# Performance work log

Measured on AMD Instinct MI355X. Metric: run time of the kernel, lower is better.

## Reference

```python
import jax, jax.numpy as jnp
import numpy as np
from jax import lax

D_MODEL, D_INNER, D_STATE, DT_RANK, KG, DCONV = 96, 96, 64, 6, 4, 3
BATCH, SEQ = 4, 16384


def setup_inputs() -> dict:
    ks = jax.random.split(jax.random.key(0), 8)
    x = jax.random.normal(ks[0], (BATCH, SEQ, D_MODEL), jnp.float32)
    in_proj_w = jax.random.normal(ks[1], (2 * D_INNER, D_MODEL), jnp.float32) * (D_MODEL ** -0.5)
    conv_w = jax.random.normal(ks[2], (D_INNER, 1, DCONV), jnp.float32) * (DCONV ** -0.5)
    x_proj_w = jax.random.normal(ks[3], (KG, DT_RANK + 2 * D_STATE, D_INNER), jnp.float32) * (D_INNER ** -0.5)
    dt_projs_w = 0.1 * jax.random.uniform(ks[4], (KG, D_INNER, DT_RANK), jnp.float32)
    out_proj_w = jax.random.normal(ks[5], (D_MODEL, D_INNER), jnp.float32) * (D_INNER ** -0.5)
    A_logs = 0.1 * jax.random.uniform(ks[6], (KG * D_INNER, D_STATE), jnp.float32)
    Ds = jnp.ones((KG * D_INNER,), jnp.float32)
    return dict(x=x, in_proj_w=in_proj_w, conv_w=conv_w, x_proj_w=x_proj_w,
                dt_projs_w=dt_projs_w, out_proj_w=out_proj_w, A_logs=A_logs, Ds=Ds)


def _forward_core(x, x_proj_w, dt_projs_w, A_logs, Ds):
    # x: (B, L, Din). 4-direction stack: [fwd, rev, fwd, rev] as in torch code.
    B, L, Din = x.shape
    x_rev = jnp.flip(x, axis=1)
    xs = jnp.stack([x, x_rev, x, x_rev], axis=1)                      # (B, K, L, Din)
    x_dbl = jnp.einsum('bkld,kcd->bklc', xs, x_proj_w)                # (B, K, L, R+2N)
    dts, Bs, Cs = jnp.split(x_dbl, [DT_RANK, DT_RANK + D_STATE], axis=-1)
    dts = jnp.einsum('bklr,kdr->bkld', dts, dt_projs_w)               # (B, K, L, Din)
    delta = jax.nn.softplus(dts)                                      # delta_bias is zeros in source
    A = -jnp.exp(A_logs).reshape(KG, D_INNER, D_STATE)                # (K, Din, N)
    D = Ds.reshape(KG, D_INNER)

    def step(h, inp):
        d, u, b, c = inp                                              # d,u:(B,K,Din)  b,c:(B,K,N)
        dA = jnp.exp(d[..., None] * A)                                # (B,K,Din,N)
        h = dA * h + (d * u)[..., None] * b[:, :, None, :]
        y = jnp.einsum('bkdn,bkn->bkd', h, c)
        return h, y

    seq = (jnp.moveaxis(delta, 2, 0), jnp.moveaxis(xs, 2, 0),
           jnp.moveaxis(Bs, 2, 0), jnp.moveaxis(Cs, 2, 0))
    h0 = jnp.zeros((B, KG, D_INNER, D_STATE), x.dtype)
    _, ys = lax.scan(step, h0, seq)                                   # (L, B, K, Din)
    ys = jnp.moveaxis(ys, 0, 2) + D[None, :, None, :] * xs            # (B, K, L, Din)
    # cross-merge: un-flip the reversed directions and sum all 4
    y = ys[:, 0] + jnp.flip(ys[:, 1], axis=1) + ys[:, 2] + jnp.flip(ys[:, 3], axis=1)
    return y                                                          # (B, L, Din)


def reference(x, in_proj_w, conv_w, x_proj_w, dt_projs_w, out_proj_w, A_logs, Ds):
    xz = x @ in_proj_w.T                                              # (B, L, 2*Din)
    xx, z = jnp.split(xz, 2, axis=-1)
    z = jax.nn.gelu(z, approximate=False)
    # depthwise conv1d over the sequence dim, 'same' padding
    pad = (DCONV - 1) // 2
    xc = lax.conv_general_dilated(xx.transpose(0, 2, 1), conv_w, (1,), [(pad, pad)],
                                  dimension_numbers=('NCH', 'OIH', 'NCH'),
                                  feature_group_count=D_INNER)        # (B, Din, L)
    xx = jax.nn.gelu(xc.transpose(0, 2, 1), approximate=False)        # (B, L, Din)
    y = _forward_core(xx, x_proj_w, dt_projs_w, A_logs, Ds)
    y = y * z
    return y @ out_proj_w.T                                           # (B, L, d_model)
```

## Files before the change

kernel.cpp:

```cpp
#include <hip/hip_runtime.h>
#include <hip/hip_bf16.h>
#include <math.h>

#define B_    4
#define L_    16384
#define DM    96
#define DI    96
#define NS    64
#define RK    6
#define KG_   4
#define CDIM  134

#define CL    512
#define NC    32
#define NWARM 64
#define STG   32

typedef float f32x2 __attribute__((ext_vector_type(2)));
typedef float f32x4 __attribute__((ext_vector_type(4)));
typedef short bf16x8 __attribute__((ext_vector_type(8)));

#if defined(__has_builtin)
# if __has_builtin(__builtin_amdgcn_exp2f)
#  define EXP2F(x) __builtin_amdgcn_exp2f(x)
# else
#  define EXP2F(x) exp2f(x)
# endif
#else
# define EXP2F(x) exp2f(x)
#endif

__device__ __forceinline__ float gelu_f(float v) {
  return 0.5f * v * (1.0f + erff(v * 0.70710678118654752f));
}

__device__ __forceinline__ unsigned short f2bf(float v) {
  __hip_bfloat16 h = __float2bfloat16(v);
  return *reinterpret_cast<unsigned short*>(&h);
}

__global__ __launch_bounds__(256) void k_front(
    const float* __restrict__ x, const float* __restrict__ w,
    const float* __restrict__ cw,
    float* __restrict__ xxc, float* __restrict__ zg)
{
  __shared__ float sx[80][100];
  __shared__ float sw[96][100];
  const int tid = threadIdx.x;
  const int lt = blockIdx.x, cs = blockIdx.y, b = blockIdx.z;
  const int l0 = lt * 64;
  const int lbase = l0 - 1;

  for (int i = tid; i < 80 * 24; i += 256) {
    const int r = i / 24, q = i % 24;
    int l = lbase + r; l = l < 0 ? 0 : (l >= L_ ? L_ - 1 : l);
    const float4 v = reinterpret_cast<const float4*>(x + ((size_t)b * L_ + l) * DM)[q];
    *reinterpret_cast<float4*>(&sx[r][q * 4]) = v;
  }
  const float* wp = w + (size_t)cs * 96 * DM;
  for (int i = tid; i < 96 * 24; i += 256) {
    const int r = i / 24, q = i % 24;
    const float4 v = reinterpret_cast<const float4*>(wp + (size_t)r * DM)[q];
    *reinterpret_cast<float4*>(&sw[r][q * 4]) = v;
  }
  __syncthreads();

  const int rg = tid & 15, cg = tid >> 4;
  float acc[5][6];
#pragma unroll
  for (int i = 0; i < 5; ++i)
#pragma unroll
    for (int jj = 0; jj < 6; ++jj) acc[i][jj] = 0.f;

  for (int d0 = 0; d0 < 96; d0 += 4) {
    float4 a[5], wv[6];
#pragma unroll
    for (int i = 0; i < 5; ++i)
      a[i] = *reinterpret_cast<const float4*>(&sx[rg + 16 * i][d0]);
#pragma unroll
    for (int jj = 0; jj < 6; ++jj)
      wv[jj] = *reinterpret_cast<const float4*>(&sw[cg + 16 * jj][d0]);
#pragma unroll
    for (int i = 0; i < 5; ++i)
#pragma unroll
      for (int jj = 0; jj < 6; ++jj)
        acc[i][jj] += a[i].x * wv[jj].x + a[i].y * wv[jj].y
                    + a[i].z * wv[jj].z + a[i].w * wv[jj].w;
  }

  __syncthreads();
  float* sprod = &sw[0][0];
#pragma unroll
  for (int i = 0; i < 5; ++i)
#pragma unroll
    for (int jj = 0; jj < 6; ++jj)
      sprod[(rg + 16 * i) * 100 + (cg + 16 * jj)] = acc[i][jj];
  __syncthreads();

  if (cs == 0) {
    float* op = xxc + ((size_t)b * L_ + l0) * DI;
    for (int i = tid; i < 64 * 24; i += 256) {
      const int ro = i / 24, q = i % 24;
      const int lo = l0 + ro;
      const float4 xm4 = *reinterpret_cast<const float4*>(&sprod[ro * 100 + q * 4]);
      const float4 x04 = *reinterpret_cast<const float4*>(&sprod[(ro + 1) * 100 + q * 4]);
      const float4 xq4 = *reinterpret_cast<const float4*>(&sprod[(ro + 2) * 100 + q * 4]);
      const float mzero = (lo > 0) ? 1.f : 0.f;
      const float qzero = (lo < L_ - 1) ? 1.f : 0.f;
      float4 o;
      {
        const int d0 = q * 4;
        const float* c = cw + d0 * 3;
        o.x = gelu_f(c[0] * xm4.x * mzero + c[1]  * x04.x + c[2]  * xq4.x * qzero);
        o.y = gelu_f(c[3] * xm4.y * mzero + c[4]  * x04.y + c[5]  * xq4.y * qzero);
        o.z = gelu_f(c[6] * xm4.z * mzero + c[7]  * x04.z + c[8]  * xq4.z * qzero);
        o.w = gelu_f(c[9] * xm4.w * mzero + c[10] * x04.w + c[11] * xq4.w * qzero);
      }
      reinterpret_cast<float4*>(op + (size_t)ro * DI)[q] = o;
    }
  } else {
    float* op = zg + ((size_t)b * L_ + l0) * DI;
    for (int i = tid; i < 64 * 24; i += 256) {
      const int ro = i / 24, q = i % 24;
      const float4 v = *reinterpret_cast<const float4*>(&sprod[(ro + 1) * 100 + q * 4]);
      float4 o;
      o.x = gelu_f(v.x); o.y = gelu_f(v.y); o.z = gelu_f(v.z); o.w = gelu_f(v.w);
      reinterpret_cast<float4*>(op + (size_t)ro * DI)[q] = o;
    }
  }
}

__global__ __launch_bounds__(256) void k_xproj(
    const float* __restrict__ xxc, const float* __restrict__ xpw,
    const float* __restrict__ dtw,
    __hip_bfloat16* __restrict__ delta, __hip_bfloat16* __restrict__ Bs,
    __hip_bfloat16* __restrict__ Cs)
{
  __shared__ __align__(16) unsigned short sxb[64][104];
  __shared__ __align__(16) unsigned short swb[144 * 104];
  __shared__ __align__(16) float sdtw[576];
  const int tid = threadIdx.x;
  const int lt = blockIdx.x, kdir = blockIdx.y, b = blockIdx.z;
  const int l0 = lt * 64;
  const bool rev = (kdir & 1) != 0;

  for (int i = tid; i < 576; i += 256) sdtw[i] = dtw[(size_t)kdir * 576 + i];

  for (int i = tid; i < 64 * 24; i += 256) {
    const int r = i / 24, q = i % 24;
    const int l = l0 + r;
    const int p = rev ? (L_ - 1 - l) : l;
    const float4 v = reinterpret_cast<const float4*>(xxc + ((size_t)b * L_ + p) * DI)[q];
    ushort4 u;
    u.x = f2bf(v.x); u.y = f2bf(v.y); u.z = f2bf(v.z); u.w = f2bf(v.w);
    *reinterpret_cast<ushort4*>(&sxb[r][q * 4]) = u;
  }
  const float* wp = xpw + (size_t)kdir * CDIM * DI;
  for (int i = tid; i < 144 * 24; i += 256) {
    const int r = i / 24, q = i % 24;
    float4 v = make_float4(0.f, 0.f, 0.f, 0.f);
    if (r < CDIM) v = reinterpret_cast<const float4*>(wp + (size_t)r * DI)[q];
    ushort4 u;
    u.x = f2bf(v.x); u.y = f2bf(v.y); u.z = f2bf(v.z); u.w = f2bf(v.w);
    *reinterpret_cast<ushort4*>(&swb[r * 104 + q * 4]) = u;
  }
  __syncthreads();

  const int wv = tid >> 6, lane = tid & 63;
  const int m0 = wv * 16;
  const int lrow = lane & 15, lkg = lane >> 4;
  f32x4 acc[9];
#pragma unroll
  for (int n = 0; n < 9; ++n) acc[n] = (f32x4){0.f, 0.f, 0.f, 0.f};

#pragma unroll
  for (int kk = 0; kk < 3; ++kk) {
    const int kbase = kk * 32 + lkg * 8;
    const bf16x8 af = *reinterpret_cast<const bf16x8*>(&sxb[m0 + lrow][kbase]);
#pragma unroll
    for (int n = 0; n < 9; ++n) {
      const bf16x8 bfm = *reinterpret_cast<const bf16x8*>(&swb[(n * 16 + lrow) * 104 + kbase]);
      acc[n] = __builtin_amdgcn_mfma_f32_16x16x32_bf16(af, bfm, acc[n], 0, 0, 0);
    }
  }
  __syncthreads();

  unsigned short* soB = swb;
  unsigned short* soC = swb + 64 * 68;
  float* sdts = reinterpret_cast<float*>(swb + 2 * 64 * 68);

  {
    const int row = m0 + lkg * 4;
#pragma unroll
    for (int n = 0; n < 9; ++n) {
      const int c = n * 16 + lrow;
#pragma unroll
      for (int reg = 0; reg < 4; ++reg) {
        const float v = acc[n][reg];
        const int rr = row + reg;
        if (c < RK)            sdts[rr * 8 + c] = v;
        else if (c < RK + NS)  soB[rr * 68 + (c - RK)] = f2bf(v);
        else if (c < CDIM)     soC[rr * 68 + (c - RK - NS)] = f2bf(v);
      }
    }
  }
  __syncthreads();

  const size_t bk = (size_t)(b * KG_ + kdir);
  {
    unsigned short* bsg = reinterpret_cast<unsigned short*>(Bs);
    unsigned short* csg = reinterpret_cast<unsigned short*>(Cs);
    const size_t nbase = (bk * L_ + l0) * NS;
    for (int i = tid; i < 64 * 16; i += 256) {
      const int r = i >> 4, q = i & 15;
      const ushort4 vb = *reinterpret_cast<const ushort4*>(&soB[r * 68 + q * 4]);
      const ushort4 vc = *reinterpret_cast<const ushort4*>(&soC[r * 68 + q * 4]);
      *reinterpret_cast<ushort4*>(bsg + nbase + (size_t)r * NS + q * 4) = vb;
      *reinterpret_cast<ushort4*>(csg + nbase + (size_t)r * NS + q * 4) = vc;
    }
  }
  {
    unsigned short* dg = reinterpret_cast<unsigned short*>(delta);
    const size_t dbase = (bk * L_ + l0) * DI;
    for (int i = tid; i < 64 * 24; i += 256) {
      const int r = i / 24, q = i - r * 24;
      const int dc0 = q * 4;
      ushort4 u;
      float o[4];
#pragma unroll
      for (int e = 0; e < 4; ++e) {
        const int dc = dc0 + e;
        float s = 0.f;
#pragma unroll
        for (int rr6 = 0; rr6 < RK; ++rr6)
          s += sdts[r * 8 + rr6] * sdtw[dc * RK + rr6];
        o[e] = (s > 20.f) ? s : log1pf(__expf(s));
      }
      u.x = f2bf(o[0]); u.y = f2bf(o[1]); u.z = f2bf(o[2]); u.w = f2bf(o[3]);
      *reinterpret_cast<ushort4*>(dg + dbase + (size_t)r * DI + dc0) = u;
    }
  }
}

__global__ __launch_bounds__(768) void k_scan(
    const float* __restrict__ xxc,
    const __hip_bfloat16* __restrict__ delta,
    const __hip_bfloat16* __restrict__ Bs,
    const __hip_bfloat16* __restrict__ Cs,
    const float* __restrict__ A_logs, const float* __restrict__ Ds,
    float* __restrict__ ysum)
{
  __shared__ __align__(16) float s_du[STG][192];
  __shared__ __align__(16) float s_u[STG][96];
  __shared__ __align__(16) float s_B[STG][64];
  __shared__ __align__(16) float s_C[STG][64];
  __shared__ __align__(16) float s_y[STG][96];
  const int tid = threadIdx.x;
  const int ci = blockIdx.x, k = blockIdx.y, b = blockIdx.z;
  const int d = tid >> 3, j = tid & 7;
  const int jn = j * 8;
  const bool rev = (k & 1) != 0;
  const float LOG2E = 1.4426950408889634f;

  const int r96 = tid / 96;
  const int c96 = tid - r96 * 96;
  const int r64 = tid >> 6;
  const int c64 = tid & 63;

  f32x2 a2[4], h[4];
#pragma unroll
  for (int p = 0; p < 4; ++p) {
    const int n = jn + 2 * p;
    a2[p].x = -__expf(A_logs[((size_t)(k * DI + d)) * NS + n])     * LOG2E;
    a2[p].y = -__expf(A_logs[((size_t)(k * DI + d)) * NS + n + 1]) * LOG2E;
    h[p].x = 0.f; h[p].y = 0.f;
  }
  const float Dc = Ds[k * DI + c96];

  const int emit0 = ci * CL;
  const int lstart = (emit0 - NWARM > 0) ? (emit0 - NWARM) : 0;
  const int lend = emit0 + CL;
  const size_t bk = (size_t)(b * KG_ + k);

  for (int s = lstart; s < lend; s += STG) {
    __syncthreads();
    {
      const size_t dbase = (bk * L_ + s) * DI;
      const int pbase = rev ? (L_ - 1 - s) : s;
      const int psgn  = rev ? -1 : 1;
      const float* ubase = xxc + ((size_t)b * L_ + pbase) * DI + c96;
#pragma unroll
      for (int it = 0; it < 4; ++it) {
        const int t = r96 + 8 * it;
        const float dl = __bfloat162float(delta[dbase + (size_t)t * DI + c96]);
        const float uu = ubase[(ptrdiff_t)psgn * t * DI];
        f32x2 v; v.x = dl; v.y = dl * uu;
        *(f32x2*)&s_du[t][2 * c96] = v;
        s_u[t][c96] = uu;
      }
      const size_t nbase = (bk * L_ + s) * NS;
#pragma unroll
      for (int it = 0; it < 3; ++it) {
        const int t = r64 + 12 * it;
        if (t < STG) {
          s_B[t][c64] = __bfloat162float(Bs[nbase + (size_t)t * NS + c64]);
          s_C[t][c64] = __bfloat162float(Cs[nbase + (size_t)t * NS + c64]);
        }
      }
    }
    __syncthreads();
    const bool emit = (s >= emit0);
#pragma unroll 8
    for (int t = 0; t < STG; ++t) {
      const f32x2 du = *(const f32x2*)&s_du[t][2 * d];
      const float dlt = du.x, bu = du.y;
      const f32x2 dlt2 = {dlt, dlt};
      const f32x2 bu2 = {bu, bu};
      const f32x4 Bv0 = *(const f32x4*)&s_B[t][jn];
      const f32x4 Bv1 = *(const f32x4*)&s_B[t][jn + 4];
      const f32x4 Cv0 = *(const f32x4*)&s_C[t][jn];
      const f32x4 Cv1 = *(const f32x4*)&s_C[t][jn + 4];
      const f32x2 bp[4] = {{Bv0.x, Bv0.y}, {Bv0.z, Bv0.w},
                           {Bv1.x, Bv1.y}, {Bv1.z, Bv1.w}};
      const f32x2 cp[4] = {{Cv0.x, Cv0.y}, {Cv0.z, Cv0.w},
                           {Cv1.x, Cv1.y}, {Cv1.z, Cv1.w}};
      f32x2 y2 = {0.f, 0.f};
#pragma unroll
      for (int p = 0; p < 4; ++p) {
        const f32x2 arg = dlt2 * a2[p];
        f32x2 e;
        e.x = EXP2F(arg.x);
        e.y = EXP2F(arg.y);
        h[p] = e * h[p] + bu2 * bp[p];
        y2 += h[p] * cp[p];
      }
      float y = y2.x + y2.y;
      y += __shfl_xor(y, 1);
      y += __shfl_xor(y, 2);
      y += __shfl_xor(y, 4);
      if (emit && j == 0) s_y[t][d] = y;
    }
    if (emit) {
      __syncthreads();
      const int pbase = rev ? (L_ - 1 - s) : s;
      const int psgn  = rev ? -1 : 1;
      float* ybase = ysum + ((size_t)b * L_ + pbase) * DI + c96;
#pragma unroll
      for (int it = 0; it < 4; ++it) {
        const int t = r96 + 8 * it;
        atomicAdd(ybase + (ptrdiff_t)psgn * t * DI,
                  fmaf(Dc, s_u[t][c96], s_y[t][c96]));
      }
    }
  }
}

__global__ __launch_bounds__(256) void k_out(
    const float* __restrict__ ysum, const float* __restrict__ zg,
    const float* __restrict__ wout, float* __restrict__ out)
{
  __shared__ float sa[64][100];
  __shared__ float sw[96][100];
  const int tid = threadIdx.x;
  const int lt = blockIdx.x, b = blockIdx.y;
  const int l0 = lt * 64;
  const size_t rbase = ((size_t)b * L_ + l0) * DI;

  for (int i = tid; i < 64 * 24; i += 256) {
    const int r = i / 24, q = i % 24;
    float4 av = reinterpret_cast<const float4*>(ysum + rbase + (size_t)r * DI)[q];
    const float4 zv = reinterpret_cast<const float4*>(zg + rbase + (size_t)r * DI)[q];
    av.x *= zv.x; av.y *= zv.y; av.z *= zv.z; av.w *= zv.w;
    *reinterpret_cast<float4*>(&sa[r][q * 4]) = av;
  }
  for (int i = tid; i < 96 * 24; i += 256) {
    const int r = i / 24, q = i % 24;
    const float4 v = reinterpret_cast<const float4*>(wout + (size_t)r * DM)[q];
    *reinterpret_cast<float4*>(&sw[r][q * 4]) = v;
  }
  __syncthreads();

  const int rg = tid & 15, cg = tid >> 4;
  float acc[4][6];
#pragma unroll
  for (int i = 0; i < 4; ++i)
#pragma unroll
    for (int jj = 0; jj < 6; ++jj) acc[i][jj] = 0.f;

  for (int d0 = 0; d0 < 96; d0 += 4) {
    float4 a[4], wv[6];
#pragma unroll
    for (int i = 0; i < 4; ++i)
      a[i] = *reinterpret_cast<const float4*>(&sa[rg + 16 * i][d0]);
#pragma unroll
    for (int jj = 0; jj < 6; ++jj)
      wv[jj] = *reinterpret_cast<const float4*>(&sw[cg + 16 * jj][d0]);
#pragma unroll
    for (int i = 0; i < 4; ++i)
#pragma unroll
      for (int jj = 0; jj < 6; ++jj)
        acc[i][jj] += a[i].x * wv[jj].x + a[i].y * wv[jj].y
                    + a[i].z * wv[jj].z + a[i].w * wv[jj].w;
  }

  __syncthreads();
  float* sout = &sw[0][0];
#pragma unroll
  for (int i = 0; i < 4; ++i)
#pragma unroll
    for (int jj = 0; jj < 6; ++jj)
      sout[(rg + 16 * i) * 100 + (cg + 16 * jj)] = acc[i][jj];
  __syncthreads();

  float* op = out + ((size_t)b * L_ + l0) * DM;
  for (int i = tid; i < 64 * 24; i += 256) {
    const int r = i / 24, q = i % 24;
    const float4 v = *reinterpret_cast<const float4*>(&sout[r * 100 + q * 4]);
    reinterpret_cast<float4*>(op + (size_t)r * DM)[q] = v;
  }
}

extern "C" void kernel_launch(void* const* d_in, const int* in_sizes, int n_in,
                              void* d_out, int out_size, void* d_ws, size_t ws_size,
                              hipStream_t stream)
{
  const float* x    = (const float*)d_in[0];
  const float* ipw  = (const float*)d_in[1];
  const float* cw   = (const float*)d_in[2];
  const float* xpw  = (const float*)d_in[3];
  const float* dtw  = (const float*)d_in[4];
  const float* opw  = (const float*)d_in[5];
  const float* alog = (const float*)d_in[6];
  const float* dsv  = (const float*)d_in[7];
  float* out = (float*)d_out;
  char* ws = (char*)d_ws;

  const size_t SZ_XZ  = (size_t)B_ * L_ * 192 * 4;
  const size_t SZ_F   = (size_t)B_ * L_ * DI * 4;
  const size_t SZ_NBF = (size_t)B_ * KG_ * L_ * NS * 2;

  __hip_bfloat16* dlt  = (__hip_bfloat16*)ws;
  float* xxc           = (float*)(ws + SZ_XZ);
  float* zgp           = (float*)(ws + SZ_XZ + SZ_F);
  __hip_bfloat16* Bsp  = (__hip_bfloat16*)(ws + SZ_XZ + 2 * SZ_F);
  __hip_bfloat16* Csp  = (__hip_bfloat16*)(ws + SZ_XZ + 2 * SZ_F + SZ_NBF);
  float* ysum          = (float*)(ws + SZ_XZ + 2 * SZ_F + 2 * SZ_NBF);

  hipMemsetAsync(ysum, 0, SZ_F, stream);
  k_front  <<<dim3(L_ / 64, 2, B_),   256, 0, stream>>>(x, ipw, cw, xxc, zgp);
  k_xproj  <<<dim3(L_ / 64, KG_, B_), 256, 0, stream>>>(xxc, xpw, dtw, dlt, Bsp, Csp);
  k_scan   <<<dim3(NC, KG_, B_),      768, 0, stream>>>(xxc, dlt, Bsp, Csp, alog, dsv, ysum);
  k_out    <<<dim3(L_ / 64, B_),      256, 0, stream>>>(ysum, zgp, opw, out);
}
```

Measured before the change: 536.9 us.

## Double-buffer scan staging with register prefetch and use bf16 MFMA in out-projection

```diff
diff --git a/kernel.cpp b/kernel.cpp
--- a/kernel.cpp
+++ b/kernel.cpp
@@ -14,7 +14,7 @@
 #define CL    512
 #define NC    32
 #define NWARM 64
-#define STG   32
+#define STG   16
 
 typedef float f32x2 __attribute__((ext_vector_type(2)));
 typedef float f32x4 __attribute__((ext_vector_type(4)));
@@ -37,6 +37,10 @@
 __device__ __forceinline__ unsigned short f2bf(float v) {
   __hip_bfloat16 h = __float2bfloat16(v);
   return *reinterpret_cast<unsigned short*>(&h);
+}
+
+__device__ __forceinline__ float bf2f(unsigned short u) {
+  return __uint_as_float(((unsigned)u) << 16);
 }
 
 __global__ __launch_bounds__(256) void k_front(
@@ -250,11 +254,10 @@
     const float* __restrict__ A_logs, const float* __restrict__ Ds,
     float* __restrict__ ysum)
 {
-  __shared__ __align__(16) float s_du[STG][192];
-  __shared__ __align__(16) float s_u[STG][96];
-  __shared__ __align__(16) float s_B[STG][64];
-  __shared__ __align__(16) float s_C[STG][64];
-  __shared__ __align__(16) float s_y[STG][96];
+  __shared__ __align__(16) float s_du[2][STG][192];
+  __shared__ __align__(16) float s_B[2][STG][64];
+  __shared__ __align__(16) float s_C[2][STG][64];
+  __shared__ __align__(16) float s_y[2][STG][96];
   const int tid = threadIdx.x;
   const int ci = blockIdx.x, k = blockIdx.y, b = blockIdx.z;
   const int d = tid >> 3, j = tid & 7;
@@ -281,45 +284,70 @@
   const int lstart = (emit0 - NWARM > 0) ? (emit0 - NWARM) : 0;
   const int lend = emit0 + CL;
   const size_t bk = (size_t)(b * KG_ + k);
-
+  const unsigned short* dltu = reinterpret_cast<const unsigned short*>(delta);
+  const unsigned short* bsu  = reinterpret_cast<const unsigned short*>(Bs);
+  const unsigned short* csu  = reinterpret_cast<const unsigned short*>(Cs);
+
+  unsigned short pf_dl[2]; float pf_u[2];
+  unsigned short pf_B[2], pf_C[2];
+
+#define LOADR(S)                                                              \
+  {                                                                           \
+    const size_t dbase_ = (bk * L_ + (S)) * DI;                               \
+    const int pb_ = rev ? (L_ - 1 - (S)) : (S);                               \
+    const int ps_ = rev ? -1 : 1;                                             \
+    const float* ub_ = xxc + ((size_t)b * L_ + pb_) * DI + c96;               \
+    _Pragma("unroll")                                                         \
+    for (int it = 0; it < 2; ++it) {                                          \
+      const int t = r96 + 8 * it;                                             \
+      pf_dl[it] = dltu[dbase_ + (size_t)t * DI + c96];                        \
+      pf_u[it]  = ub_[(ptrdiff_t)ps_ * t * DI];                               \
+    }                                                                         \
+    const size_t nbase_ = (bk * L_ + (S)) * NS;                               \
+    _Pragma("unroll")                                                         \
+    for (int it = 0; it < 2; ++it) {                                          \
+      const int t = r64 + 12 * it;                                            \
+      if (t < STG) {                                                          \
+        pf_B[it] = bsu[nbase_ + (size_t)t * NS + c64];                        \
+        pf_C[it] = csu[nbase_ + (size_t)t * NS + c64];                        \
+      }                                                                       \
+    }                                                                         \
+  }
+
+  LOADR(lstart);
+  int pb = 0;
   for (int s = lstart; s < lend; s += STG) {
+#pragma unroll
+    for (int it = 0; it < 2; ++it) {
+      const int t = r96 + 8 * it;
+      const float dl = bf2f(pf_dl[it]);
+      const float uu = pf_u[it];
+      f32x2 v; v.x = dl; v.y = dl * uu;
+      *(f32x2*)&s_du[pb][t][2 * c96] = v;
+      s_y[pb][t][c96] = Dc * uu;
+    }
+#pragma unroll
+    for (int it = 0; it < 2; ++it) {
+      const int t = r64 + 12 * it;
+      if (t < STG) {
+        s_B[pb][t][c64] = bf2f(pf_B[it]);
+        s_C[pb][t][c64] = bf2f(pf_C[it]);
+      }
+    }
     __syncthreads();
-    {
-      const size_t dbase = (bk * L_ + s) * DI;
-      const int pbase = rev ? (L_ - 1 - s) : s;
-      const int psgn  = rev ? -1 : 1;
-      const float* ubase = xxc + ((size_t)b * L_ + pbase) * DI + c96;
-#pragma unroll
-      for (int it = 0; it < 4; ++it) {
-        const int t = r96 + 8 * it;
-        const float dl = __bfloat162float(delta[dbase + (size_t)t * DI + c96]);
-        const float uu = ubase[(ptrdiff_t)psgn * t * DI];
-        f32x2 v; v.x = dl; v.y = dl * uu;
-        *(f32x2*)&s_du[t][2 * c96] = v;
-        s_u[t][c96] = uu;
-      }
-      const size_t nbase = (bk * L_ + s) * NS;
-#pragma unroll
-      for (int it = 0; it < 3; ++it) {
-        const int t = r64 + 12 * it;
-        if (t < STG) {
-          s_B[t][c64] = __bfloat162float(Bs[nbase + (size_t)t * NS + c64]);
-          s_C[t][c64] = __bfloat162float(Cs[nbase + (size_t)t * NS + c64]);
-        }
-      }
-    }
-    __syncthreads();
+    if (s + STG < lend) LOADR(s + STG);
+
     const bool emit = (s >= emit0);
 #pragma unroll 8
     for (int t = 0; t < STG; ++t) {
-      const f32x2 du = *(const f32x2*)&s_du[t][2 * d];
+      const f32x2 du = *(const f32x2*)&s_du[pb][t][2 * d];
       const float dlt = du.x, bu = du.y;
       const f32x2 dlt2 = {dlt, dlt};
       const f32x2 bu2 = {bu, bu};
-      const f32x4 Bv0 = *(const f32x4*)&s_B[t][jn];
-      const f32x4 Bv1 = *(const f32x4*)&s_B[t][jn + 4];
-      const f32x4 Cv0 = *(const f32x4*)&s_C[t][jn];
-      const f32x4 Cv1 = *(const f32x4*)&s_C[t][jn + 4];
+      const f32x4 Bv0 = *(const f32x4*)&s_B[pb][t][jn];
+      const f32x4 Bv1 = *(const f32x4*)&s_B[pb][t][jn + 4];
+      const f32x4 Cv0 = *(const f32x4*)&s_C[pb][t][jn];
+      const f32x4 Cv1 = *(const f32x4*)&s_C[pb][t][jn + 4];
       const f32x2 bp[4] = {{Bv0.x, Bv0.y}, {Bv0.z, Bv0.w},
                            {Bv1.x, Bv1.y}, {Bv1.z, Bv1.w}};
       const f32x2 cp[4] = {{Cv0.x, Cv0.y}, {Cv0.z, Cv0.w},
@@ -338,29 +366,31 @@
       y += __shfl_xor(y, 1);
       y += __shfl_xor(y, 2);
       y += __shfl_xor(y, 4);
-      if (emit && j == 0) s_y[t][d] = y;
-    }
+      if (emit && j == 0) atomicAdd(&s_y[pb][t][d], y);
+    }
+    __syncthreads();
     if (emit) {
-      __syncthreads();
       const int pbase = rev ? (L_ - 1 - s) : s;
       const int psgn  = rev ? -1 : 1;
       float* ybase = ysum + ((size_t)b * L_ + pbase) * DI + c96;
 #pragma unroll
-      for (int it = 0; it < 4; ++it) {
+      for (int it = 0; it < 2; ++it) {
         const int t = r96 + 8 * it;
-        atomicAdd(ybase + (ptrdiff_t)psgn * t * DI,
-                  fmaf(Dc, s_u[t][c96], s_y[t][c96]));
-      }
-    }
-  }
+        atomicAdd(ybase + (ptrdiff_t)psgn * t * DI, s_y[pb][t][c96]);
+      }
+    }
+    pb ^= 1;
+  }
+#undef LOADR
 }
 
 __global__ __launch_bounds__(256) void k_out(
     const float* __restrict__ ysum, const float* __restrict__ zg,
     const float* __restrict__ wout, float* __restrict__ out)
 {
-  __shared__ float sa[64][100];
-  __shared__ float sw[96][100];
+  __shared__ __align__(16) char smem[64 * 104 * 2 + 96 * 104 * 2];
+  unsigned short* sab = reinterpret_cast<unsigned short*>(smem);
+  unsigned short* swb = reinterpret_cast<unsigned short*>(smem + 64*104*2);
   const int tid = threadIdx.x;
   const int lt = blockIdx.x, b = blockIdx.y;
   const int l0 = lt * 64;
@@ -370,46 +400,50 @@
     const int r = i / 24, q = i % 24;
     float4 av = reinterpret_cast<const float4*>(ysum + rbase + (size_t)r * DI)[q];
     const float4 zv = reinterpret_cast<const float4*>(zg + rbase + (size_t)r * DI)[q];
-    av.x *= zv.x; av.y *= zv.y; av.z *= zv.z; av.w *= zv.w;
-    *reinterpret_cast<float4*>(&sa[r][q * 4]) = av;
+    ushort4 u;
+    u.x = f2bf(av.x * zv.x); u.y = f2bf(av.y * zv.y);
+    u.z = f2bf(av.z * zv.z); u.w = f2bf(av.w * zv.w);
+    *reinterpret_cast<ushort4*>(&sab[r * 104 + q * 4]) = u;
   }
   for (int i = tid; i < 96 * 24; i += 256) {
     const int r = i / 24, q = i % 24;
     const float4 v = reinterpret_cast<const float4*>(wout + (size_t)r * DM)[q];
-    *reinterpret_cast<float4*>(&sw[r][q * 4]) = v;
-  }
-  __syncthreads();
-
-  const int rg = tid & 15, cg = tid >> 4;
-  float acc[4][6];
-#pragma unroll
-  for (int i = 0; i < 4; ++i)
-#pragma unroll
-    for (int jj = 0; jj < 6; ++jj) acc[i][jj] = 0.f;
-
-  for (int d0 = 0; d0 < 96; d0 += 4) {
-    float4 a[4], wv[6];
-#pragma unroll
-    for (int i = 0; i < 4; ++i)
-      a[i] = *reinterpret_cast<const float4*>(&sa[rg + 16 * i][d0]);
-#pragma unroll
-    for (int jj = 0; jj < 6; ++jj)
-      wv[jj] = *reinterpret_cast<const float4*>(&sw[cg + 16 * jj][d0]);
-#pragma unroll
-    for (int i = 0; i < 4; ++i)
-#pragma unroll
-      for (int jj = 0; jj < 6; ++jj)
-        acc[i][jj] += a[i].x * wv[jj].x + a[i].y * wv[jj].y
-                    + a[i].z * wv[jj].z + a[i].w * wv[jj].w;
-  }
-
-  __syncthreads();
-  float* sout = &sw[0][0];
-#pragma unroll
-  for (int i = 0; i < 4; ++i)
-#pragma unroll
-    for (int jj = 0; jj < 6; ++jj)
-      sout[(rg + 16 * i) * 100 + (cg + 16 * jj)] = acc[i][jj];
+    ushort4 u;
+    u.x = f2bf(v.x); u.y = f2bf(v.y); u.z = f2bf(v.z); u.w = f2bf(v.w);
+    *reinterpret_cast<ushort4*>(&swb[r * 104 + q * 4]) = u;
+  }
+  __syncthreads();
+
+  const int wv = tid >> 6, lane = tid & 63;
+  const int m0 = wv * 16;
+  const int lrow = lane & 15, lkg = lane >> 4;
+  f32x4 acc[6];
+#pragma unroll
+  for (int n = 0; n < 6; ++n) acc[n] = (f32x4){0.f, 0.f, 0.f, 0.f};
+
+#pragma unroll
+  for (int kk = 0; kk < 3; ++kk) {
+    const int kbase = kk * 32 + lkg * 8;
+    const bf16x8 af = *reinterpret_cast<const bf16x8*>(&sab[(m0 + lrow) * 104 + kbase]);
+#pragma unroll
+    for (int n = 0; n < 6; ++n) {
+      const bf16x8 bfm = *reinterpret_cast<const bf16x8*>(&swb[(n * 16 + lrow) * 104 + kbase]);
+      acc[n] = __builtin_amdgcn_mfma_f32_16x16x32_bf16(af, bfm, acc[n], 0, 0, 0);
+    }
+  }
+  __syncthreads();
+
+  float* sout = reinterpret_cast<float*>(smem);
+  {
+    const int row = m0 + lkg * 4;
+#pragma unroll
+    for (int n = 0; n < 6; ++n) {
+      const int c = n * 16 + lrow;
+#pragma unroll
+      for (int reg = 0; reg < 4; ++reg)
+        sout[(row + reg) * 100 + c] = acc[n][reg];
+    }
+  }
   __syncthreads();
 
   float* op = out + ((size_t)b * L_ + l0) * DM;
```

New measurement: 611.5 us. 1.14x slower.
